# Kernel tuning notes

Hardware: AMD Instinct MI355X
Metric: run time of the kernel (lower is better)

Reference implementation:

```python
import jax, jax.numpy as jnp
import numpy as np

NUM_CLASSES = 19
NUM_PROTO = 10
PROJ_DIM = 720
SK_ITERS = 3
SK_EPS = 0.05
MEAN_GAMMA = 0.999
N = 4 * 128 * 256  # b*h*w = 131072 pixels


def l2n(v, axis=-1):
    return v / jnp.maximum(jnp.linalg.norm(v, axis=axis, keepdims=True), 1e-12)


def layer_norm(v, g, b, eps=1e-5):
    mu = jnp.mean(v, axis=-1, keepdims=True)
    var = jnp.var(v, axis=-1, keepdims=True)
    return (v - mu) / jnp.sqrt(var + eps) * g + b


def _safe_div(a, d):
    return jnp.where(d > 0, a / jnp.where(d > 0, d, 1.0), 0.0)


def setup_inputs() -> dict:
    key = jax.random.key(0)
    k0, k1, k2 = jax.random.split(key, 3)
    x = jax.random.normal(k0, (N, PROJ_DIM), jnp.float32)
    gt_seg = jax.random.randint(k1, (N,), 0, NUM_CLASSES)
    prototypes = 0.02 * jax.random.normal(k2, (NUM_CLASSES, NUM_PROTO, PROJ_DIM), jnp.float32)
    return {
        "x": x,
        "prototypes": prototypes,
        "fn_g": jnp.ones((PROJ_DIM,), jnp.float32),
        "fn_b": jnp.zeros((PROJ_DIM,), jnp.float32),
        "mn_g": jnp.ones((NUM_CLASSES,), jnp.float32),
        "mn_b": jnp.zeros((NUM_CLASSES,), jnp.float32),
        "pn_g": jnp.ones((NUM_CLASSES * NUM_PROTO,), jnp.float32),
        "pn_b": jnp.zeros((NUM_CLASSES * NUM_PROTO,), jnp.float32),
        "gt_seg": gt_seg,
    }


def reference(x, prototypes, fn_g, fn_b, mn_g, mn_b, pn_g, pn_b, gt_seg):
    n = x.shape[0]
    # feat_norm + l2 normalize pixel embeddings; prototypes l2-normalized in-place
    _c = l2n(layer_norm(x, fn_g, fn_b))
    protos = l2n(prototypes)  # [k, m, d]

    # cosine similarity: [n, k, m]
    sim = jnp.einsum("nd,kmd->nkm", _c, protos)
    out_seg = layer_norm(jnp.max(sim, axis=-1), mn_g, mn_b)          # [n, k]
    contrast_logits = layer_norm(sim.reshape(n, -1), pn_g, pn_b)     # [n, k*m]

    # ---- prototype learning (class-masked Sinkhorn, vectorized over classes) ----
    pred = jnp.argmax(out_seg, axis=-1)
    correct = (gt_seg == pred).astype(sim.dtype)                     # [n]
    row_mask = (gt_seg[None, :] == jnp.arange(NUM_CLASSES)[:, None]).astype(sim.dtype)  # [k, n]
    Bk = row_mask.sum(axis=1)                                        # pixels per class

    q0 = jnp.transpose(sim, (1, 0, 2))                               # [k, n, m]
    L = jnp.exp(q0 / SK_EPS) * row_mask[..., None]
    L = _safe_div(L, L.sum(axis=(1, 2), keepdims=True))
    for _ in range(SK_ITERS):
        # normalize over pixels (per prototype), then over prototypes (per pixel)
        L = _safe_div(L, L.sum(axis=1, keepdims=True)) / NUM_PROTO
        L = _safe_div(L, L.sum(axis=2, keepdims=True))
        L = _safe_div(L, Bk[:, None, None])
    L = L * Bk[:, None, None]

    idx = jnp.argmax(L, axis=-1)                                     # [k, n] hard assignment
    onehot = jax.nn.one_hot(idx, NUM_PROTO, dtype=sim.dtype) * row_mask[..., None]
    m_q = onehot * correct[None, :, None]                            # [k, n, m]
    n_km = m_q.sum(axis=1)                                           # [k, m]

    # f = m_q^T @ c_q per class (c_q = _c masked by correct; boolean mask squared == mask)
    f = l2n(jnp.einsum("knm,nd->kmd", m_q, _c))
    valid = (n_km != 0) & (n_km.sum(axis=1, keepdims=True) > 0)      # [k, m]
    updated = MEAN_GAMMA * protos + (1.0 - MEAN_GAMMA) * f
    protos_new = l2n(jnp.where(valid[..., None], updated, protos))

    # proto_target: per-pixel selected prototype offset into the flat codebook
    idx_pix = idx[gt_seg, jnp.arange(n)]
    proto_target = idx_pix.astype(jnp.float32) + NUM_PROTO * gt_seg.astype(jnp.float32)

    return out_seg, contrast_logits, proto_target, protos_new
```

## Files before the change

### kernel.cpp

```cpp
#include <hip/hip_runtime.h>
#include <math.h>

#define NCLS 19
#define NPROTO 10
#define KM 190
#define KMP 192
#define D 720
#define BM 64
#define CHK 16
#define NCHK 45

typedef __bf16 bf16x8 __attribute__((ext_vector_type(8)));
typedef float f32x16 __attribute__((ext_vector_type(16)));

__device__ __forceinline__ float wred_sum(float v) {
#pragma unroll
  for (int o = 32; o > 0; o >>= 1) v += __shfl_xor(v, o, 64);
  return v;
}
__device__ __forceinline__ float wred_max(float v) {
#pragma unroll
  for (int o = 32; o > 0; o >>= 1) v = fmaxf(v, __shfl_xor(v, o, 64));
  return v;
}
__device__ __forceinline__ double wred_sumd(double v) {
#pragma unroll
  for (int o = 32; o > 0; o >>= 1) v += __shfl_xor(v, o, 64);
  return v;
}

__device__ __forceinline__ ushort bf_hi(float v, float& hf) {
  const uint u = __float_as_uint(v);
  const uint r = (u + 0x7FFFu + ((u >> 16) & 1u)) >> 16;
  hf = __uint_as_float(r << 16);
  return (ushort)r;
}

__global__ void prep_gb(const float* __restrict__ fg, const float* __restrict__ fb,
                        float* __restrict__ G2, float* __restrict__ GB,
                        float* __restrict__ C3) {
  const int t = threadIdx.x;
  float cg = 0.f, cgb = 0.f, cb = 0.f;
  for (int d2 = t; d2 < D; d2 += 256) {
    const float g = fg[d2], b = fb[d2];
    G2[d2] = g * g;
    GB[d2] = g * b;
    cg = fmaf(g, g, cg);
    cgb = fmaf(g, b, cgb);
    cb = fmaf(b, b, cb);
  }
  __shared__ float red[3][4];
  cg = wred_sum(cg); cgb = wred_sum(cgb); cb = wred_sum(cb);
  const int w = t >> 6, lane = t & 63;
  if (lane == 0) { red[0][w] = cg; red[1][w] = cgb; red[2][w] = cb; }
  __syncthreads();
  if (t == 0) {
    C3[0] = red[0][0] + red[0][1] + red[0][2] + red[0][3];
    C3[1] = red[1][0] + red[1][1] + red[1][2] + red[1][3];
    C3[2] = red[2][0] + red[2][1] + red[2][2] + red[2][3];
  }
}

__global__ void proto_prep(const float* __restrict__ pr, const float* __restrict__ fg,
                           const float* __restrict__ fb, ushort* __restrict__ pgtb,
                           float* __restrict__ Av, float* __restrict__ Bv) {
  const int j = blockIdx.x, lane = threadIdx.x;
  if (j >= KM) {
#pragma unroll
    for (int jj = 0; jj < 12; ++jj) {
      const int d2 = lane + 64 * jj;
      if (d2 < D) {
        const int c = d2 >> 4, kb = (d2 >> 3) & 1, e = d2 & 7;
        const size_t b0 = (size_t)c * 6144 + (size_t)kb * KMP * 8 + (size_t)j * 8 + e;
        pgtb[b0] = 0;
        pgtb[b0 + 2 * KMP * 8] = 0;
      }
    }
    if (lane == 0) { Av[j] = 0.f; Bv[j] = 0.f; }
    return;
  }
  float pv[12];
  float sp = 0.f;
#pragma unroll
  for (int jj = 0; jj < 12; ++jj) {
    const int d2 = lane + 64 * jj;
    pv[jj] = (d2 < D) ? pr[(size_t)j * D + d2] : 0.f;
    sp = fmaf(pv[jj], pv[jj], sp);
  }
  sp = wred_sum(sp);
  const float ip = 1.f / fmaxf(sqrtf(sp), 1e-12f);
  float sa = 0.f, sb = 0.f;
#pragma unroll
  for (int jj = 0; jj < 12; ++jj) {
    const int d2 = lane + 64 * jj;
    if (d2 < D) {
      const float ph = pv[jj] * ip;
      const float g = fg[d2], b = fb[d2];
      const float val = g * ph;
      float hf, dummy;
      const ushort h = bf_hi(val, hf);
      const ushort l = bf_hi(val - hf, dummy);
      const int c = d2 >> 4, kb = (d2 >> 3) & 1, e = d2 & 7;
      const size_t b0 = (size_t)c * 6144 + (size_t)kb * KMP * 8 + (size_t)j * 8 + e;
      pgtb[b0] = h;
      pgtb[b0 + 2 * KMP * 8] = l;
      sa = fmaf(g, ph, sa);
      sb = fmaf(b, ph, sb);
    }
  }
  sa = wred_sum(sa); sb = wred_sum(sb);
  if (lane == 0) { Av[j] = sa; Bv[j] = sb; }
}

__global__ __launch_bounds__(256, 3) void gemm_main(
    const float* __restrict__ x, const ushort* __restrict__ pgtb,
    const float* __restrict__ Av, const float* __restrict__ Bv,
    const float* __restrict__ G2, const float* __restrict__ GB,
    const float* __restrict__ C3, const int* __restrict__ gt,
    float* __restrict__ out_seg, float* __restrict__ contrast,
    float* __restrict__ se, int* __restrict__ flags,
    const float* __restrict__ mn_g, const float* __restrict__ mn_b,
    const float* __restrict__ pn_g, const float* __restrict__ pn_b, int N) {
  __shared__ __align__(16) union {
    struct {
      ushort X[2][2][2][BM][8];
      ushort P[2][2][2][KMP][8];
    } g;
    float ST[5][4][BM];
    float SIM[BM][KMP];
  } U;
  __shared__ float A_s[KMP], B_s[KMP];
  __shared__ float PGn[KMP], PBn[KMP];
  __shared__ float MGn[32], MBn[32];
  __shared__ float MU[BM], RS[BM], IL[BM];

  const int t = threadIdx.x;
  const int n0 = blockIdx.x * BM;
  const int w = t >> 6, lane = t & 63;
  const int wm = w >> 1, wn = w & 1;
  const int l31 = lane & 31, lhi = lane >> 5;
  const int pix = t & 63, q = t >> 6;

  if (t < KMP) {
    A_s[t] = Av[t]; B_s[t] = Bv[t];
    PGn[t] = (t < KM) ? pn_g[t] : 0.f;
    PBn[t] = (t < KM) ? pn_b[t] : 0.f;
  }
  if (t < NCLS) { MGn[t] = mn_g[t]; MBn[t] = mn_b[t]; }

  f32x16 acc[3];
#pragma unroll
  for (int nt = 0; nt < 3; ++nt)
#pragma unroll
    for (int e = 0; e < 16; ++e) acc[nt][e] = 0.f;

  float s0 = 0.f, qq = 0.f, s1 = 0.f, s2 = 0.f, s3 = 0.f;

  const float* xrow = x + (size_t)(n0 + pix) * D + 4 * q;
  const int kb0 = q >> 1, e0 = (q & 1) * 4;

  auto stageX = [&](int nb, const float4& xv, const float4& g2, const float4& gb) {
    const float vs4[4] = {xv.x, xv.y, xv.z, xv.w};
    const float g2s[4] = {g2.x, g2.y, g2.z, g2.w};
    const float gbs[4] = {gb.x, gb.y, gb.z, gb.w};
    ushort h[4], l[4];
#pragma unroll
    for (int e = 0; e < 4; ++e) {
      const float v = vs4[e];
      float hf, dm;
      h[e] = bf_hi(v, hf);
      l[e] = bf_hi(v - hf, dm);
      s0 += v;
      const float xx = v * v;
      qq += xx;
      s1 = fmaf(v, g2s[e], s1);
      s2 = fmaf(xx, g2s[e], s2);
      s3 = fmaf(v, gbs[e], s3);
    }
    *(ushort4*)&U.g.X[nb][0][kb0][pix][e0] = make_ushort4(h[0], h[1], h[2], h[3]);
    *(ushort4*)&U.g.X[nb][1][kb0][pix][e0] = make_ushort4(l[0], l[1], l[2], l[3]);
  };

  auto mfmaStep = [&](int bf) {
    const int row = 32 * wm + l31;
    const bf16x8 ah = *reinterpret_cast<const bf16x8*>(&U.g.X[bf][0][lhi][row][0]);
    const bf16x8 al = *reinterpret_cast<const bf16x8*>(&U.g.X[bf][1][lhi][row][0]);
    bf16x8 bh[3], bl[3];
#pragma unroll
    for (int nt = 0; nt < 3; ++nt) {
      const int col = 96 * wn + 32 * nt + l31;
      bh[nt] = *reinterpret_cast<const bf16x8*>(&U.g.P[bf][0][lhi][col][0]);
      bl[nt] = *reinterpret_cast<const bf16x8*>(&U.g.P[bf][1][lhi][col][0]);
    }
#pragma unroll
    for (int nt = 0; nt < 3; ++nt)
      acc[nt] = __builtin_amdgcn_mfma_f32_32x32x16_bf16(ah, bh[nt], acc[nt], 0, 0, 0);
#pragma unroll
    for (int nt = 0; nt < 3; ++nt)
      acc[nt] = __builtin_amdgcn_mfma_f32_32x32x16_bf16(ah, bl[nt], acc[nt], 0, 0, 0);
#pragma unroll
    for (int nt = 0; nt < 3; ++nt)
      acc[nt] = __builtin_amdgcn_mfma_f32_32x32x16_bf16(al, bh[nt], acc[nt], 0, 0, 0);
  };

  {
    const uint4* ps = (const uint4*)pgtb;
    const uint4 p0 = ps[t], p1 = ps[t + 256], p2 = ps[t + 512];
    const float4 xv = *(const float4*)xrow;
    const float4 g2 = *(const float4*)&G2[4 * q];
    const float4 gb = *(const float4*)&GB[4 * q];
    uint4* pd = (uint4*)&U.g.P[0][0][0][0][0];
    pd[t] = p0; pd[t + 256] = p1; pd[t + 512] = p2;
    stageX(0, xv, g2, gb);
  }
  __syncthreads();

  for (int c = 0; c < NCHK; ++c) {
    const int buf = c & 1;
    uint4 p0, p1, p2;
    float4 xv, g2, gb;
    const bool pf = (c + 1 < NCHK);
    if (pf) {
      const uint4* ps = (const uint4*)(pgtb + (size_t)(c + 1) * 6144);
      p0 = ps[t]; p1 = ps[t + 256]; p2 = ps[t + 512];
      xv = *(const float4*)(xrow + (c + 1) * CHK);
      const int d0 = (c + 1) * CHK + 4 * q;
      g2 = *(const float4*)&G2[d0];
      gb = *(const float4*)&GB[d0];
    }
    mfmaStep(buf);
    if (pf) {
      uint4* pd = (uint4*)&U.g.P[buf ^ 1][0][0][0][0];
      pd[t] = p0; pd[t + 256] = p1; pd[t + 512] = p2;
      stageX(buf ^ 1, xv, g2, gb);
    }
    __syncthreads();
  }

  U.ST[0][q][pix] = s0;
  U.ST[1][q][pix] = qq;
  U.ST[2][q][pix] = s1;
  U.ST[3][q][pix] = s2;
  U.ST[4][q][pix] = s3;
  __syncthreads();
  if (t < BM) {
    float S0 = 0.f, Q = 0.f, S1 = 0.f, S2 = 0.f, S3 = 0.f;
#pragma unroll
    for (int s = 0; s < 4; ++s) {
      S0 += U.ST[0][s][t];
      Q += U.ST[1][s][t];
      S1 += U.ST[2][s][t];
      S2 += U.ST[3][s][t];
      S3 += U.ST[4][s][t];
    }
    const float Cgg = C3[0], Cgb = C3[1], Cbb = C3[2];
    const float mu = S0 / 720.f;
    const float var = Q / 720.f - mu * mu;
    const float rs = 1.f / sqrtf(var + 1e-5f);
    const float L2v = rs * rs * (S2 - 2.f * mu * S1 + mu * mu * Cgg) +
                      2.f * rs * (S3 - mu * Cgb) + Cbb;
    MU[t] = mu;
    RS[t] = rs;
    IL[t] = 1.f / fmaxf(sqrtf(fmaxf(L2v, 0.f)), 1e-12f);
  }
  __syncthreads();

#pragma unroll
  for (int nt = 0; nt < 3; ++nt) {
    const int col = 96 * wn + 32 * nt + l31;
    const float aC = A_s[col], bC = B_s[col];
#pragma unroll
    for (int rg = 0; rg < 16; ++rg) {
      const int pr = 32 * wm + (rg & 3) + 8 * (rg >> 2) + 4 * lhi;
      U.SIM[pr][col] = (RS[pr] * (acc[nt][rg] - MU[pr] * aC) + bC) * IL[pr];
    }
  }
  __syncthreads();

  const int j0 = lane, j1 = lane + 64, j2 = lane + 128;
  const bool ok2 = (j2 < KM);
  for (int pi = 0; pi < 16; ++pi) {
    const int px = w * 16 + pi;
    const int n = n0 + px;
    const float sv0 = U.SIM[px][j0];
    const float sv1 = U.SIM[px][j1];
    const float sv2 = ok2 ? U.SIM[px][j2] : 0.f;
    float sum = sv0 + sv1 + sv2;
    sum = wred_sum(sum);
    const float mu = sum / 190.f;
    const float d0v = sv0 - mu, d1v = sv1 - mu, d2v = ok2 ? (sv2 - mu) : 0.f;
    float vs = d0v * d0v + d1v * d1v + d2v * d2v;
    vs = wred_sum(vs);
    const float rstd = 1.f / sqrtf(vs / 190.f + 1e-5f);
    contrast[(size_t)n * KM + j0] = d0v * rstd * PGn[j0] + PBn[j0];
    contrast[(size_t)n * KM + j1] = d1v * rstd * PGn[j1] + PBn[j1];
    if (ok2) contrast[(size_t)n * KM + j2] = d2v * rstd * PGn[j2] + PBn[j2];
    const int g0 = gt[n];
    const int b10 = g0 * 10;
    if (j0 >= b10 && j0 < b10 + 10) se[(size_t)n * 10 + (j0 - b10)] = sv0;
    if (j1 >= b10 && j1 < b10 + 10) se[(size_t)n * 10 + (j1 - b10)] = sv1;
    if (ok2 && j2 >= b10 && j2 < b10 + 10) se[(size_t)n * 10 + (j2 - b10)] = sv2;
    float mx = -3.0e38f;
    if (lane < NCLS) {
      const float* row = &U.SIM[px][lane * 10];
#pragma unroll
      for (int m2 = 0; m2 < 10; ++m2) mx = fmaxf(mx, row[m2]);
    }
    float s19 = wred_sum(lane < NCLS ? mx : 0.f);
    const float mu19 = s19 / 19.f;
    const float dv = (lane < NCLS) ? (mx - mu19) : 0.f;
    float v19 = wred_sum(dv * dv);
    const float rs19 = 1.f / sqrtf(v19 / 19.f + 1e-5f);
    float key = -3.0e38f;
    if (lane < NCLS) {
      const float os = dv * rs19 * MGn[lane] + MBn[lane];
      out_seg[(size_t)n * NCLS + lane] = os;
      key = os;
    }
    const float kmax = wred_max(key);
    const unsigned long long bm = __ballot(key == kmax);
    const int pred = __ffsll((unsigned long long)bm) - 1;
    if (lane == 0) flags[n] = (pred == g0) ? 1 : 0;
  }
}

__global__ void sk_colsum(const float* __restrict__ se, const int* __restrict__ gt,
                          const float* __restrict__ u, float* __restrict__ partials,
                          int iter, int nblk, int N) {
  __shared__ float Sl[KMP];
  const int t = threadIdx.x;
  if (t < KMP) Sl[t] = 0.f;
  __syncthreads();
  const int n = blockIdx.x * 256 + t;
  if (n < N) {
    const int b10 = gt[n] * 10;
    float e[10];
#pragma unroll
    for (int m = 0; m < 10; ++m) e[m] = expf(se[(size_t)n * 10 + m] / 0.05f);
    float a = 1.f;
    if (iter > 0) {
      float s = 0.f;
#pragma unroll
      for (int m = 0; m < 10; ++m) s += e[m] * u[b10 + m];
      a = (s > 0.f) ? 1.f / s : 0.f;
    }
#pragma unroll
    for (int m = 0; m < 10; ++m) atomicAdd(&Sl[b10 + m], a * e[m]);
  }
  __syncthreads();
  if (t < KM) partials[(size_t)t * nblk + blockIdx.x] = Sl[t];
}

__global__ void sk_reduce(const float* __restrict__ partials, float* __restrict__ u,
                          int nblk) {
  const int j = blockIdx.x, lane = threadIdx.x;
  double s = 0.0;
  for (int b = lane; b < nblk; b += 64) s += (double)partials[(size_t)j * nblk + b];
  s = wred_sumd(s);
  if (lane == 0) u[j] = (s > 0.0) ? (float)(1.0 / (10.0 * s)) : 0.f;
}

__global__ void sk_final(const float* __restrict__ se, const int* __restrict__ gt,
                         const float* __restrict__ u, const int* __restrict__ flags,
                         float* __restrict__ ptgt, int* __restrict__ list,
                         int* __restrict__ cnt, int* __restrict__ n_km, int N) {
  const int n = blockIdx.x * 256 + threadIdx.x;
  if (n >= N) return;
  const int g0 = gt[n], b10 = g0 * 10;
  float best = -1.f;
  int bi = 0;
#pragma unroll
  for (int m = 0; m < 10; ++m) {
    const float v = expf(se[(size_t)n * 10 + m] / 0.05f) * u[b10 + m];
    if (v > best) { best = v; bi = m; }
  }
  ptgt[n] = (float)(bi + 10 * g0);
  if (flags[n]) {
    atomicAdd(&n_km[b10 + bi], 1);
    const int p = atomicAdd(cnt, 1);
    list[p] = n | (bi << 20) | (g0 << 24);
  }
}

__global__ void f_accum(const float* __restrict__ x, const float* __restrict__ fg,
                        const float* __restrict__ fb, const int* __restrict__ list,
                        const int* __restrict__ cnt, float* __restrict__ f) {
  const int lane = threadIdx.x & 63;
  const int wid = (blockIdx.x * blockDim.x + threadIdx.x) >> 6;
  const int nw = (gridDim.x * blockDim.x) >> 6;
  const int total = *cnt;
  for (int i = wid; i < total; i += nw) {
    const int packed = list[i];
    const int n = packed & 0xFFFFF;
    const int m = (packed >> 20) & 0xF;
    const int k = (packed >> 24) & 0x1F;
    float xv[12];
    float s0 = 0.f, q = 0.f;
#pragma unroll
    for (int jj = 0; jj < 12; ++jj) {
      const int d2 = lane + 64 * jj;
      xv[jj] = (d2 < D) ? x[(size_t)n * D + d2] : 0.f;
      s0 += xv[jj];
      q = fmaf(xv[jj], xv[jj], q);
    }
    s0 = wred_sum(s0);
    q = wred_sum(q);
    const float mu = s0 / 720.f;
    const float var = q / 720.f - mu * mu;
    const float rs = 1.f / sqrtf(var + 1e-5f);
    float cv[12];
    float l2 = 0.f;
#pragma unroll
    for (int jj = 0; jj < 12; ++jj) {
      const int d2 = lane + 64 * jj;
      if (d2 < D) {
        cv[jj] = (xv[jj] - mu) * rs * fg[d2] + fb[d2];
        l2 = fmaf(cv[jj], cv[jj], l2);
      } else {
        cv[jj] = 0.f;
      }
    }
    l2 = wred_sum(l2);
    const float il = 1.f / fmaxf(sqrtf(l2), 1e-12f);
    float* frow = &f[(size_t)(k * 10 + m) * D];
#pragma unroll
    for (int jj = 0; jj < 12; ++jj) {
      const int d2 = lane + 64 * jj;
      if (d2 < D) atomicAdd(&frow[d2], cv[jj] * il);
    }
  }
}

__global__ void protos_out(const float* __restrict__ pr, const float* __restrict__ f,
                           const int* __restrict__ n_km, float* __restrict__ out) {
  const int j = blockIdx.x, lane = threadIdx.x;
  float pv[12], fv[12];
  float sp = 0.f, sf = 0.f;
#pragma unroll
  for (int jj = 0; jj < 12; ++jj) {
    const int d2 = lane + 64 * jj;
    pv[jj] = (d2 < D) ? pr[(size_t)j * D + d2] : 0.f;
    fv[jj] = (d2 < D) ? f[(size_t)j * D + d2] : 0.f;
    sp = fmaf(pv[jj], pv[jj], sp);
    sf = fmaf(fv[jj], fv[jj], sf);
  }
  sp = wred_sum(sp);
  sf = wred_sum(sf);
  const float ip = 1.f / fmaxf(sqrtf(sp), 1e-12f);
  const float iff = 1.f / fmaxf(sqrtf(sf), 1e-12f);
  const bool valid = n_km[j] > 0;
  float vv[12];
  float sv = 0.f;
#pragma unroll
  for (int jj = 0; jj < 12; ++jj) {
    const float ph = pv[jj] * ip;
    vv[jj] = valid ? (0.999f * ph + 0.001f * (fv[jj] * iff)) : ph;
    sv = fmaf(vv[jj], vv[jj], sv);
  }
  sv = wred_sum(sv);
  const float ivv = 1.f / fmaxf(sqrtf(sv), 1e-12f);
#pragma unroll
  for (int jj = 0; jj < 12; ++jj) {
    const int d2 = lane + 64 * jj;
    if (d2 < D) out[(size_t)j * D + d2] = vv[jj] * ivv;
  }
}

extern "C" void kernel_launch(void* const* d_in, const int* in_sizes, int n_in,
                              void* d_out, int out_size, void* d_ws, size_t ws_size,
                              hipStream_t stream) {
  const float* x = (const float*)d_in[0];
  const float* protos = (const float*)d_in[1];
  const float* fn_g = (const float*)d_in[2];
  const float* fn_b = (const float*)d_in[3];
  const float* mn_g = (const float*)d_in[4];
  const float* mn_b = (const float*)d_in[5];
  const float* pn_g = (const float*)d_in[6];
  const float* pn_b = (const float*)d_in[7];
  const int* gt = (const int*)d_in[8];
  const int N = in_sizes[0] / D;

  float* out_seg = (float*)d_out;
  float* contrast = out_seg + (size_t)N * NCLS;
  float* ptgt = contrast + (size_t)N * KM;
  float* pnew = ptgt + (size_t)N;

  char* ws = (char*)d_ws;
  size_t off = 0;
  auto alloc = [&](size_t bytes) {
    char* p = ws + off;
    off = (off + bytes + 255) & ~(size_t)255;
    return p;
  };
  const int nblk = (N + 255) / 256;
  ushort* pgtb = (ushort*)alloc((size_t)NCHK * 6144 * 2);
  float* Av = (float*)alloc(KMP * 4);
  float* Bv = (float*)alloc(KMP * 4);
  float* G2 = (float*)alloc(D * 4);
  float* GB = (float*)alloc(D * 4);
  float* C3 = (float*)alloc(4 * 4);
  float* se = (float*)alloc((size_t)N * 10 * 4);
  float* partials = (float*)alloc((size_t)KM * nblk * 4);
  float* u = (float*)alloc(KMP * 4);
  float* f = (float*)alloc((size_t)KM * D * 4);
  int* n_km = (int*)alloc(KMP * 4);
  int* flags = (int*)alloc((size_t)N * 4);
  int* list = (int*)alloc((size_t)N * 4);
  int* cnt = (int*)alloc(256);

  hipMemsetAsync(f, 0, (size_t)KM * D * 4, stream);
  hipMemsetAsync(n_km, 0, KMP * 4, stream);
  hipMemsetAsync(cnt, 0, 4, stream);

  prep_gb<<<1, 256, 0, stream>>>(fn_g, fn_b, G2, GB, C3);
  proto_prep<<<KMP, 64, 0, stream>>>(protos, fn_g, fn_b, pgtb, Av, Bv);
  gemm_main<<<N / BM, 256, 0, stream>>>(x, pgtb, Av, Bv, G2, GB, C3, gt, out_seg,
                                        contrast, se, flags, mn_g, mn_b, pn_g,
                                        pn_b, N);
  for (int it = 0; it < 3; ++it) {
    sk_colsum<<<nblk, 256, 0, stream>>>(se, gt, u, partials, it, nblk, N);
    sk_reduce<<<KM, 64, 0, stream>>>(partials, u, nblk);
  }
  sk_final<<<nblk, 256, 0, stream>>>(se, gt, u, flags, ptgt, list, cnt, n_km, N);
  f_accum<<<256, 256, 0, stream>>>(x, fn_g, fn_b, list, cnt, f);
  protos_out<<<KM, 64, 0, stream>>>(protos, f, n_km, pnew);
}
```

Baseline: 861.5 us.

## Restructure pipeline: larger GEMM tile, split epilogue, fused Sinkhorn and prototype update

The GEMM tile grows to 128 rows per block with two accumulator row groups per warp, and the similarity matrix is written straight to global memory instead of being staged in shared memory. The layer-norm epilogue moves into a separate kernel that reads those rows back. The Sinkhorn colsum/reduce/final launches are merged into one per-class kernel with 1024 threads, and f_accum plus protos_out become a single per-prototype gather kernel that reuses stored per-pixel mu/rstd/inverse-norm values. This cuts launch count, atomics and the recomputation of x statistics, but adds an extra global round trip of the 190-wide similarity rows. It also leaves only 19 blocks for the Sinkhorn passes, each scanning all of gt.

```diff
diff --git a/kernel.cpp b/kernel.cpp
--- a/kernel.cpp
+++ b/kernel.cpp
@@ -6,7 +6,7 @@
 #define KM 190
 #define KMP 192
 #define D 720
-#define BM 64
+#define BM 128
 #define CHK 16
 #define NCHK 45
 
@@ -36,35 +36,30 @@
   return (ushort)r;
 }
 
-__global__ void prep_gb(const float* __restrict__ fg, const float* __restrict__ fb,
-                        float* __restrict__ G2, float* __restrict__ GB,
-                        float* __restrict__ C3) {
-  const int t = threadIdx.x;
-  float cg = 0.f, cgb = 0.f, cb = 0.f;
-  for (int d2 = t; d2 < D; d2 += 256) {
-    const float g = fg[d2], b = fb[d2];
-    G2[d2] = g * g;
-    GB[d2] = g * b;
-    cg = fmaf(g, g, cg);
-    cgb = fmaf(g, b, cgb);
-    cb = fmaf(b, b, cb);
-  }
-  __shared__ float red[3][4];
-  cg = wred_sum(cg); cgb = wred_sum(cgb); cb = wred_sum(cb);
-  const int w = t >> 6, lane = t & 63;
-  if (lane == 0) { red[0][w] = cg; red[1][w] = cgb; red[2][w] = cb; }
-  __syncthreads();
-  if (t == 0) {
-    C3[0] = red[0][0] + red[0][1] + red[0][2] + red[0][3];
-    C3[1] = red[1][0] + red[1][1] + red[1][2] + red[1][3];
-    C3[2] = red[2][0] + red[2][1] + red[2][2] + red[2][3];
-  }
-}
-
-__global__ void proto_prep(const float* __restrict__ pr, const float* __restrict__ fg,
-                           const float* __restrict__ fb, ushort* __restrict__ pgtb,
-                           float* __restrict__ Av, float* __restrict__ Bv) {
+__global__ void prep_all(const float* __restrict__ pr, const float* __restrict__ fg,
+                         const float* __restrict__ fb, ushort* __restrict__ pgtb,
+                         float* __restrict__ Av, float* __restrict__ Bv,
+                         float* __restrict__ G2, float* __restrict__ GB,
+                         float* __restrict__ C3) {
   const int j = blockIdx.x, lane = threadIdx.x;
+  if (j == KMP) {
+    float cg = 0.f, cgb = 0.f, cb = 0.f;
+#pragma unroll
+    for (int jj = 0; jj < 12; ++jj) {
+      const int d2 = lane + 64 * jj;
+      if (d2 < D) {
+        const float g = fg[d2], b = fb[d2];
+        G2[d2] = g * g;
+        GB[d2] = g * b;
+        cg = fmaf(g, g, cg);
+        cgb = fmaf(g, b, cgb);
+        cb = fmaf(b, b, cb);
+      }
+    }
+    cg = wred_sum(cg); cgb = wred_sum(cgb); cb = wred_sum(cb);
+    if (lane == 0) { C3[0] = cg; C3[1] = cgb; C3[2] = cb; }
+    return;
+  }
   if (j >= KM) {
 #pragma unroll
     for (int jj = 0; jj < 12; ++jj) {
@@ -116,22 +111,17 @@
     const float* __restrict__ x, const ushort* __restrict__ pgtb,
     const float* __restrict__ Av, const float* __restrict__ Bv,
     const float* __restrict__ G2, const float* __restrict__ GB,
-    const float* __restrict__ C3, const int* __restrict__ gt,
-    float* __restrict__ out_seg, float* __restrict__ contrast,
-    float* __restrict__ se, int* __restrict__ flags,
-    const float* __restrict__ mn_g, const float* __restrict__ mn_b,
-    const float* __restrict__ pn_g, const float* __restrict__ pn_b, int N) {
+    const float* __restrict__ C3, float* __restrict__ simC,
+    float* __restrict__ MUg, float* __restrict__ RSg, float* __restrict__ ILg,
+    int N) {
   __shared__ __align__(16) union {
     struct {
       ushort X[2][2][2][BM][8];
       ushort P[2][2][2][KMP][8];
     } g;
-    float ST[5][4][BM];
-    float SIM[BM][KMP];
+    float ST[5][2][BM];
   } U;
   __shared__ float A_s[KMP], B_s[KMP];
-  __shared__ float PGn[KMP], PBn[KMP];
-  __shared__ float MGn[32], MBn[32];
   __shared__ float MU[BM], RS[BM], IL[BM];
 
   const int t = threadIdx.x;
@@ -139,170 +129,189 @@
   const int w = t >> 6, lane = t & 63;
   const int wm = w >> 1, wn = w & 1;
   const int l31 = lane & 31, lhi = lane >> 5;
-  const int pix = t & 63, q = t >> 6;
-
-  if (t < KMP) {
-    A_s[t] = Av[t]; B_s[t] = Bv[t];
-    PGn[t] = (t < KM) ? pn_g[t] : 0.f;
-    PBn[t] = (t < KM) ? pn_b[t] : 0.f;
-  }
-  if (t < NCLS) { MGn[t] = mn_g[t]; MBn[t] = mn_b[t]; }
-
-  f32x16 acc[3];
-#pragma unroll
-  for (int nt = 0; nt < 3; ++nt)
-#pragma unroll
-    for (int e = 0; e < 16; ++e) acc[nt][e] = 0.f;
+  const int p = t & 127, h = t >> 7;
+
+  if (t < KMP) { A_s[t] = Av[t]; B_s[t] = Bv[t]; }
+
+  f32x16 acc[2][3];
+#pragma unroll
+  for (int mr = 0; mr < 2; ++mr)
+#pragma unroll
+    for (int nt = 0; nt < 3; ++nt)
+#pragma unroll
+      for (int e = 0; e < 16; ++e) acc[mr][nt][e] = 0.f;
 
   float s0 = 0.f, qq = 0.f, s1 = 0.f, s2 = 0.f, s3 = 0.f;
 
-  const float* xrow = x + (size_t)(n0 + pix) * D + 4 * q;
-  const int kb0 = q >> 1, e0 = (q & 1) * 4;
-
-  auto stageX = [&](int nb, const float4& xv, const float4& g2, const float4& gb) {
-    const float vs4[4] = {xv.x, xv.y, xv.z, xv.w};
-    const float g2s[4] = {g2.x, g2.y, g2.z, g2.w};
-    const float gbs[4] = {gb.x, gb.y, gb.z, gb.w};
-    ushort h[4], l[4];
-#pragma unroll
-    for (int e = 0; e < 4; ++e) {
-      const float v = vs4[e];
+  const float* xrow = x + (size_t)(n0 + p) * D + 8 * h;
+
+  auto stageX = [&](int nb, int c, const float4& xa, const float4& xb) {
+    const int d0 = c * CHK + 8 * h;
+    const float4 g2a = *(const float4*)&G2[d0];
+    const float4 g2b = *(const float4*)&G2[d0 + 4];
+    const float4 gba = *(const float4*)&GB[d0];
+    const float4 gbb = *(const float4*)&GB[d0 + 4];
+    const float v[8] = {xa.x, xa.y, xa.z, xa.w, xb.x, xb.y, xb.z, xb.w};
+    const float gg[8] = {g2a.x, g2a.y, g2a.z, g2a.w, g2b.x, g2b.y, g2b.z, g2b.w};
+    const float gv[8] = {gba.x, gba.y, gba.z, gba.w, gbb.x, gbb.y, gbb.z, gbb.w};
+    ushort hh[8], ll[8];
+#pragma unroll
+    for (int e = 0; e < 8; ++e) {
+      const float xv = v[e];
       float hf, dm;
-      h[e] = bf_hi(v, hf);
-      l[e] = bf_hi(v - hf, dm);
-      s0 += v;
-      const float xx = v * v;
+      hh[e] = bf_hi(xv, hf);
+      ll[e] = bf_hi(xv - hf, dm);
+      s0 += xv;
+      const float xx = xv * xv;
       qq += xx;
-      s1 = fmaf(v, g2s[e], s1);
-      s2 = fmaf(xx, g2s[e], s2);
-      s3 = fmaf(v, gbs[e], s3);
-    }
-    *(ushort4*)&U.g.X[nb][0][kb0][pix][e0] = make_ushort4(h[0], h[1], h[2], h[3]);
-    *(ushort4*)&U.g.X[nb][1][kb0][pix][e0] = make_ushort4(l[0], l[1], l[2], l[3]);
+      s1 = fmaf(xv, gg[e], s1);
+      s2 = fmaf(xx, gg[e], s2);
+      s3 = fmaf(xv, gv[e], s3);
+    }
+    *(uint4*)&U.g.X[nb][0][h][p][0] =
+        make_uint4((uint)hh[0] | ((uint)hh[1] << 16), (uint)hh[2] | ((uint)hh[3] << 16),
+                   (uint)hh[4] | ((uint)hh[5] << 16), (uint)hh[6] | ((uint)hh[7] << 16));
+    *(uint4*)&U.g.X[nb][1][h][p][0] =
+        make_uint4((uint)ll[0] | ((uint)ll[1] << 16), (uint)ll[2] | ((uint)ll[3] << 16),
+                   (uint)ll[4] | ((uint)ll[5] << 16), (uint)ll[6] | ((uint)ll[7] << 16));
   };
 
   auto mfmaStep = [&](int bf) {
-    const int row = 32 * wm + l31;
-    const bf16x8 ah = *reinterpret_cast<const bf16x8*>(&U.g.X[bf][0][lhi][row][0]);
-    const bf16x8 al = *reinterpret_cast<const bf16x8*>(&U.g.X[bf][1][lhi][row][0]);
-    bf16x8 bh[3], bl[3];
+    const int row0 = 64 * wm + l31;
+    const bf16x8 ah0 = *reinterpret_cast<const bf16x8*>(&U.g.X[bf][0][lhi][row0][0]);
+    const bf16x8 ah1 = *reinterpret_cast<const bf16x8*>(&U.g.X[bf][0][lhi][row0 + 32][0]);
+    const bf16x8 al0 = *reinterpret_cast<const bf16x8*>(&U.g.X[bf][1][lhi][row0][0]);
+    const bf16x8 al1 = *reinterpret_cast<const bf16x8*>(&U.g.X[bf][1][lhi][row0 + 32][0]);
 #pragma unroll
     for (int nt = 0; nt < 3; ++nt) {
       const int col = 96 * wn + 32 * nt + l31;
-      bh[nt] = *reinterpret_cast<const bf16x8*>(&U.g.P[bf][0][lhi][col][0]);
-      bl[nt] = *reinterpret_cast<const bf16x8*>(&U.g.P[bf][1][lhi][col][0]);
-    }
-#pragma unroll
-    for (int nt = 0; nt < 3; ++nt)
-      acc[nt] = __builtin_amdgcn_mfma_f32_32x32x16_bf16(ah, bh[nt], acc[nt], 0, 0, 0);
-#pragma unroll
-    for (int nt = 0; nt < 3; ++nt)
-      acc[nt] = __builtin_amdgcn_mfma_f32_32x32x16_bf16(ah, bl[nt], acc[nt], 0, 0, 0);
-#pragma unroll
-    for (int nt = 0; nt < 3; ++nt)
-      acc[nt] = __builtin_amdgcn_mfma_f32_32x32x16_bf16(al, bh[nt], acc[nt], 0, 0, 0);
+      const bf16x8 bh = *reinterpret_cast<const bf16x8*>(&U.g.P[bf][0][lhi][col][0]);
+      const bf16x8 bl = *reinterpret_cast<const bf16x8*>(&U.g.P[bf][1][lhi][col][0]);
+      acc[0][nt] = __builtin_amdgcn_mfma_f32_32x32x16_bf16(ah0, bh, acc[0][nt], 0, 0, 0);
+      acc[1][nt] = __builtin_amdgcn_mfma_f32_32x32x16_bf16(ah1, bh, acc[1][nt], 0, 0, 0);
+      acc[0][nt] = __builtin_amdgcn_mfma_f32_32x32x16_bf16(ah0, bl, acc[0][nt], 0, 0, 0);
+      acc[1][nt] = __builtin_amdgcn_mfma_f32_32x32x16_bf16(ah1, bl, acc[1][nt], 0, 0, 0);
+      acc[0][nt] = __builtin_amdgcn_mfma_f32_32x32x16_bf16(al0, bh, acc[0][nt], 0, 0, 0);
+      acc[1][nt] = __builtin_amdgcn_mfma_f32_32x32x16_bf16(al1, bh, acc[1][nt], 0, 0, 0);
+    }
   };
 
   {
     const uint4* ps = (const uint4*)pgtb;
     const uint4 p0 = ps[t], p1 = ps[t + 256], p2 = ps[t + 512];
-    const float4 xv = *(const float4*)xrow;
-    const float4 g2 = *(const float4*)&G2[4 * q];
-    const float4 gb = *(const float4*)&GB[4 * q];
+    const float4 xa = *(const float4*)xrow;
+    const float4 xb = *(const float4*)(xrow + 4);
     uint4* pd = (uint4*)&U.g.P[0][0][0][0][0];
     pd[t] = p0; pd[t + 256] = p1; pd[t + 512] = p2;
-    stageX(0, xv, g2, gb);
+    stageX(0, 0, xa, xb);
   }
   __syncthreads();
 
   for (int c = 0; c < NCHK; ++c) {
     const int buf = c & 1;
+    const bool pf = (c + 1 < NCHK);
     uint4 p0, p1, p2;
-    float4 xv, g2, gb;
-    const bool pf = (c + 1 < NCHK);
+    float4 xa, xb;
     if (pf) {
       const uint4* ps = (const uint4*)(pgtb + (size_t)(c + 1) * 6144);
       p0 = ps[t]; p1 = ps[t + 256]; p2 = ps[t + 512];
-      xv = *(const float4*)(xrow + (c + 1) * CHK);
-      const int d0 = (c + 1) * CHK + 4 * q;
-      g2 = *(const float4*)&G2[d0];
-      gb = *(const float4*)&GB[d0];
+      xa = *(const float4*)(xrow + (c + 1) * CHK);
+      xb = *(const float4*)(xrow + (c + 1) * CHK + 4);
     }
     mfmaStep(buf);
     if (pf) {
       uint4* pd = (uint4*)&U.g.P[buf ^ 1][0][0][0][0];
       pd[t] = p0; pd[t + 256] = p1; pd[t + 512] = p2;
-      stageX(buf ^ 1, xv, g2, gb);
+      stageX(buf ^ 1, c + 1, xa, xb);
     }
     __syncthreads();
   }
 
-  U.ST[0][q][pix] = s0;
-  U.ST[1][q][pix] = qq;
-  U.ST[2][q][pix] = s1;
-  U.ST[3][q][pix] = s2;
-  U.ST[4][q][pix] = s3;
+  U.ST[0][h][p] = s0;
+  U.ST[1][h][p] = qq;
+  U.ST[2][h][p] = s1;
+  U.ST[3][h][p] = s2;
+  U.ST[4][h][p] = s3;
   __syncthreads();
   if (t < BM) {
-    float S0 = 0.f, Q = 0.f, S1 = 0.f, S2 = 0.f, S3 = 0.f;
-#pragma unroll
-    for (int s = 0; s < 4; ++s) {
-      S0 += U.ST[0][s][t];
-      Q += U.ST[1][s][t];
-      S1 += U.ST[2][s][t];
-      S2 += U.ST[3][s][t];
-      S3 += U.ST[4][s][t];
-    }
+    const float S0 = U.ST[0][0][t] + U.ST[0][1][t];
+    const float Q = U.ST[1][0][t] + U.ST[1][1][t];
+    const float S1 = U.ST[2][0][t] + U.ST[2][1][t];
+    const float S2 = U.ST[3][0][t] + U.ST[3][1][t];
+    const float S3 = U.ST[4][0][t] + U.ST[4][1][t];
     const float Cgg = C3[0], Cgb = C3[1], Cbb = C3[2];
     const float mu = S0 / 720.f;
     const float var = Q / 720.f - mu * mu;
     const float rs = 1.f / sqrtf(var + 1e-5f);
     const float L2v = rs * rs * (S2 - 2.f * mu * S1 + mu * mu * Cgg) +
                       2.f * rs * (S3 - mu * Cgb) + Cbb;
-    MU[t] = mu;
-    RS[t] = rs;
-    IL[t] = 1.f / fmaxf(sqrtf(fmaxf(L2v, 0.f)), 1e-12f);
+    const float il = 1.f / fmaxf(sqrtf(fmaxf(L2v, 0.f)), 1e-12f);
+    MU[t] = mu; RS[t] = rs; IL[t] = il;
+    MUg[n0 + t] = mu; RSg[n0 + t] = rs; ILg[n0 + t] = il;
   }
   __syncthreads();
 
+  float aC[3], bC[3];
 #pragma unroll
   for (int nt = 0; nt < 3; ++nt) {
     const int col = 96 * wn + 32 * nt + l31;
-    const float aC = A_s[col], bC = B_s[col];
+    aC[nt] = A_s[col];
+    bC[nt] = B_s[col];
+  }
+#pragma unroll
+  for (int mr = 0; mr < 2; ++mr)
 #pragma unroll
     for (int rg = 0; rg < 16; ++rg) {
-      const int pr = 32 * wm + (rg & 3) + 8 * (rg >> 2) + 4 * lhi;
-      U.SIM[pr][col] = (RS[pr] * (acc[nt][rg] - MU[pr] * aC) + bC) * IL[pr];
-    }
-  }
+      const int r = 64 * wm + 32 * mr + (rg & 3) + 8 * (rg >> 2) + 4 * lhi;
+      const float mu = MU[r], rs = RS[r], il = IL[r];
+#pragma unroll
+      for (int nt = 0; nt < 3; ++nt) {
+        const int col = 96 * wn + 32 * nt + l31;
+        if (col < KM)
+          simC[(size_t)(n0 + r) * KM + col] =
+              (rs * (acc[mr][nt][rg] - mu * aC[nt]) + bC[nt]) * il;
+      }
+    }
+}
+
+__global__ __launch_bounds__(256) void epilogue(
+    float* __restrict__ co, const int* __restrict__ gt,
+    float* __restrict__ out_seg, float* __restrict__ se, int* __restrict__ flags,
+    const float* __restrict__ mn_g, const float* __restrict__ mn_b,
+    const float* __restrict__ pn_g, const float* __restrict__ pn_b, int N) {
+  __shared__ float PGn[KMP], PBn[KMP], MGn[32], MBn[32];
+  __shared__ float rowbuf[4][KMP];
+  const int t = threadIdx.x, w = t >> 6, lane = t & 63;
+  if (t < KM) { PGn[t] = pn_g[t]; PBn[t] = pn_b[t]; }
+  if (t < NCLS) { MGn[t] = mn_g[t]; MBn[t] = mn_b[t]; }
   __syncthreads();
-
+  const int n0 = blockIdx.x * 64;
   const int j0 = lane, j1 = lane + 64, j2 = lane + 128;
   const bool ok2 = (j2 < KM);
   for (int pi = 0; pi < 16; ++pi) {
-    const int px = w * 16 + pi;
-    const int n = n0 + px;
-    const float sv0 = U.SIM[px][j0];
-    const float sv1 = U.SIM[px][j1];
-    const float sv2 = ok2 ? U.SIM[px][j2] : 0.f;
-    float sum = sv0 + sv1 + sv2;
-    sum = wred_sum(sum);
+    const int n = n0 + w * 16 + pi;
+    float* crow = &co[(size_t)n * KM];
+    const float sv0 = crow[j0];
+    const float sv1 = crow[j1];
+    const float sv2 = ok2 ? crow[j2] : 0.f;
+    float sum = wred_sum(sv0 + sv1 + sv2);
     const float mu = sum / 190.f;
     const float d0v = sv0 - mu, d1v = sv1 - mu, d2v = ok2 ? (sv2 - mu) : 0.f;
-    float vs = d0v * d0v + d1v * d1v + d2v * d2v;
-    vs = wred_sum(vs);
+    float vs = wred_sum(d0v * d0v + d1v * d1v + d2v * d2v);
     const float rstd = 1.f / sqrtf(vs / 190.f + 1e-5f);
-    contrast[(size_t)n * KM + j0] = d0v * rstd * PGn[j0] + PBn[j0];
-    contrast[(size_t)n * KM + j1] = d1v * rstd * PGn[j1] + PBn[j1];
-    if (ok2) contrast[(size_t)n * KM + j2] = d2v * rstd * PGn[j2] + PBn[j2];
-    const int g0 = gt[n];
-    const int b10 = g0 * 10;
+    rowbuf[w][j0] = sv0;
+    rowbuf[w][j1] = sv1;
+    if (ok2) rowbuf[w][j2] = sv2;
+    const int g0 = gt[n], b10 = g0 * 10;
     if (j0 >= b10 && j0 < b10 + 10) se[(size_t)n * 10 + (j0 - b10)] = sv0;
     if (j1 >= b10 && j1 < b10 + 10) se[(size_t)n * 10 + (j1 - b10)] = sv1;
     if (ok2 && j2 >= b10 && j2 < b10 + 10) se[(size_t)n * 10 + (j2 - b10)] = sv2;
+    crow[j0] = d0v * rstd * PGn[j0] + PBn[j0];
+    crow[j1] = d1v * rstd * PGn[j1] + PBn[j1];
+    if (ok2) crow[j2] = d2v * rstd * PGn[j2] + PBn[j2];
     float mx = -3.0e38f;
     if (lane < NCLS) {
-      const float* row = &U.SIM[px][lane * 10];
+      const float* row = &rowbuf[w][lane * 10];
 #pragma unroll
       for (int m2 = 0; m2 < 10; ++m2) mx = fmaxf(mx, row[m2]);
     }
@@ -324,146 +333,139 @@
   }
 }
 
-__global__ void sk_colsum(const float* __restrict__ se, const int* __restrict__ gt,
-                          const float* __restrict__ u, float* __restrict__ partials,
-                          int iter, int nblk, int N) {
-  __shared__ float Sl[KMP];
-  const int t = threadIdx.x;
-  if (t < KMP) Sl[t] = 0.f;
+__global__ __launch_bounds__(1024) void sk_all(
+    const float* __restrict__ se, const int* __restrict__ gt,
+    const int* __restrict__ flags, float* __restrict__ ptgt,
+    int* __restrict__ list, int* __restrict__ cnt, int N) {
+  const int k = blockIdx.x;
+  const int t = threadIdx.x, w = t >> 6, lane = t & 63;
+  __shared__ double CS[16][10];
+  __shared__ float u_s[10];
+  for (int pass = 0; pass < 3; ++pass) {
+    double cs[10];
+#pragma unroll
+    for (int m = 0; m < 10; ++m) cs[m] = 0.0;
+    for (int n = t; n < N; n += 1024) {
+      if (gt[n] != k) continue;
+      float e[10];
+      const float2* sp2 = (const float2*)&se[(size_t)n * 10];
+#pragma unroll
+      for (int m2 = 0; m2 < 5; ++m2) {
+        const float2 v = sp2[m2];
+        e[2 * m2] = expf(v.x / 0.05f);
+        e[2 * m2 + 1] = expf(v.y / 0.05f);
+      }
+      float a = 1.f;
+      if (pass > 0) {
+        float s = 0.f;
+#pragma unroll
+        for (int m = 0; m < 10; ++m) s += e[m] * u_s[m];
+        a = (s > 0.f) ? 1.f / s : 0.f;
+      }
+#pragma unroll
+      for (int m = 0; m < 10; ++m) cs[m] += (double)(a * e[m]);
+    }
+#pragma unroll
+    for (int m = 0; m < 10; ++m) cs[m] = wred_sumd(cs[m]);
+    if (lane == 0)
+#pragma unroll
+      for (int m = 0; m < 10; ++m) CS[w][m] = cs[m];
+    __syncthreads();
+    if (t < 10) {
+      double s = 0.0;
+#pragma unroll
+      for (int ww = 0; ww < 16; ++ww) s += CS[ww][t];
+      u_s[t] = (s > 0.0) ? (float)(1.0 / (10.0 * s)) : 0.f;
+    }
+    __syncthreads();
+  }
+  for (int n = t; n < N; n += 1024) {
+    if (gt[n] != k) continue;
+    float best = -1.f;
+    int bi = 0;
+#pragma unroll
+    for (int m = 0; m < 10; ++m) {
+      const float v = expf(se[(size_t)n * 10 + m] / 0.05f) * u_s[m];
+      if (v > best) { best = v; bi = m; }
+    }
+    ptgt[n] = (float)(bi + 10 * k);
+    if (flags[n]) {
+      const int pos = atomicAdd(cnt, 1);
+      list[pos] = n | (bi << 20) | (k << 24);
+    }
+  }
+}
+
+__global__ __launch_bounds__(256) void proto_update(
+    const float* __restrict__ pr, const float* __restrict__ x,
+    const float* __restrict__ fg, const float* __restrict__ fb,
+    const float* __restrict__ MUg, const float* __restrict__ RSg,
+    const float* __restrict__ ILg, const int* __restrict__ list,
+    const int* __restrict__ cnt, float* __restrict__ out) {
+  const int j = blockIdx.x;
+  const int t = threadIdx.x, w = t >> 6, lane = t & 63;
+  const int tag = ((j / 10) << 4) | (j % 10);
+  const int d0 = t, d1 = t + 256, d2 = t + 512;
+  const bool has2 = (d2 < D);
+  const float fg0 = fg[d0], fb0 = fb[d0];
+  const float fg1 = fg[d1], fb1 = fb[d1];
+  const float fg2 = has2 ? fg[d2] : 0.f, fb2 = has2 ? fb[d2] : 0.f;
+  float fa0 = 0.f, fa1 = 0.f, fa2 = 0.f;
+  __shared__ int nlist[4096];
+  __shared__ int nmatch;
+  __shared__ float RP[4], RF[4], RV[4];
+  const int total = *cnt;
+  int hits = 0;
+  for (int base = 0; base < total; base += 4096) {
+    const int hi = min(base + 4096, total);
+    if (t == 0) nmatch = 0;
+    __syncthreads();
+    for (int i = base + t; i < hi; i += 256) {
+      const int pk = list[i];
+      if ((pk >> 20) == tag) {
+        const int pos = atomicAdd(&nmatch, 1);
+        nlist[pos] = pk & 0xFFFFF;
+      }
+    }
+    __syncthreads();
+    const int nm = nmatch;
+    hits += nm;
+    for (int ii = 0; ii < nm; ++ii) {
+      const int n = nlist[ii];
+      const float mu = MUg[n], rs = RSg[n], il = ILg[n];
+      const float* xr = &x[(size_t)n * D];
+      fa0 += ((xr[d0] - mu) * rs * fg0 + fb0) * il;
+      fa1 += ((xr[d1] - mu) * rs * fg1 + fb1) * il;
+      if (has2) fa2 += ((xr[d2] - mu) * rs * fg2 + fb2) * il;
+    }
+    __syncthreads();
+  }
+  const float pv0 = pr[(size_t)j * D + d0];
+  const float pv1 = pr[(size_t)j * D + d1];
+  const float pv2 = has2 ? pr[(size_t)j * D + d2] : 0.f;
+  float sp = pv0 * pv0 + pv1 * pv1 + pv2 * pv2;
+  float sf = fa0 * fa0 + fa1 * fa1 + fa2 * fa2;
+  sp = wred_sum(sp); sf = wred_sum(sf);
+  if (lane == 0) { RP[w] = sp; RF[w] = sf; }
   __syncthreads();
-  const int n = blockIdx.x * 256 + t;
-  if (n < N) {
-    const int b10 = gt[n] * 10;
-    float e[10];
-#pragma unroll
-    for (int m = 0; m < 10; ++m) e[m] = expf(se[(size_t)n * 10 + m] / 0.05f);
-    float a = 1.f;
-    if (iter > 0) {
-      float s = 0.f;
-#pragma unroll
-      for (int m = 0; m < 10; ++m) s += e[m] * u[b10 + m];
-      a = (s > 0.f) ? 1.f / s : 0.f;
-    }
-#pragma unroll
-    for (int m = 0; m < 10; ++m) atomicAdd(&Sl[b10 + m], a * e[m]);
-  }
-  __syncthreads();
-  if (t < KM) partials[(size_t)t * nblk + blockIdx.x] = Sl[t];
-}
-
-__global__ void sk_reduce(const float* __restrict__ partials, float* __restrict__ u,
-                          int nblk) {
-  const int j = blockIdx.x, lane = threadIdx.x;
-  double s = 0.0;
-  for (int b = lane; b < nblk; b += 64) s += (double)partials[(size_t)j * nblk + b];
-  s = wred_sumd(s);
-  if (lane == 0) u[j] = (s > 0.0) ? (float)(1.0 / (10.0 * s)) : 0.f;
-}
-
-__global__ void sk_final(const float* __restrict__ se, const int* __restrict__ gt,
-                         const float* __restrict__ u, const int* __restrict__ flags,
-                         float* __restrict__ ptgt, int* __restrict__ list,
-                         int* __restrict__ cnt, int* __restrict__ n_km, int N) {
-  const int n = blockIdx.x * 256 + threadIdx.x;
-  if (n >= N) return;
-  const int g0 = gt[n], b10 = g0 * 10;
-  float best = -1.f;
-  int bi = 0;
-#pragma unroll
-  for (int m = 0; m < 10; ++m) {
-    const float v = expf(se[(size_t)n * 10 + m] / 0.05f) * u[b10 + m];
-    if (v > best) { best = v; bi = m; }
-  }
-  ptgt[n] = (float)(bi + 10 * g0);
-  if (flags[n]) {
-    atomicAdd(&n_km[b10 + bi], 1);
-    const int p = atomicAdd(cnt, 1);
-    list[p] = n | (bi << 20) | (g0 << 24);
-  }
-}
-
-__global__ void f_accum(const float* __restrict__ x, const float* __restrict__ fg,
-                        const float* __restrict__ fb, const int* __restrict__ list,
-                        const int* __restrict__ cnt, float* __restrict__ f) {
-  const int lane = threadIdx.x & 63;
-  const int wid = (blockIdx.x * blockDim.x + threadIdx.x) >> 6;
-  const int nw = (gridDim.x * blockDim.x) >> 6;
-  const int total = *cnt;
-  for (int i = wid; i < total; i += nw) {
-    const int packed = list[i];
-    const int n = packed & 0xFFFFF;
-    const int m = (packed >> 20) & 0xF;
-    const int k = (packed >> 24) & 0x1F;
-    float xv[12];
-    float s0 = 0.f, q = 0.f;
-#pragma unroll
-    for (int jj = 0; jj < 12; ++jj) {
-      const int d2 = lane + 64 * jj;
-      xv[jj] = (d2 < D) ? x[(size_t)n * D + d2] : 0.f;
-      s0 += xv[jj];
-      q = fmaf(xv[jj], xv[jj], q);
-    }
-    s0 = wred_sum(s0);
-    q = wred_sum(q);
-    const float mu = s0 / 720.f;
-    const float var = q / 720.f - mu * mu;
-    const float rs = 1.f / sqrtf(var + 1e-5f);
-    float cv[12];
-    float l2 = 0.f;
-#pragma unroll
-    for (int jj = 0; jj < 12; ++jj) {
-      const int d2 = lane + 64 * jj;
-      if (d2 < D) {
-        cv[jj] = (xv[jj] - mu) * rs * fg[d2] + fb[d2];
-        l2 = fmaf(cv[jj], cv[jj], l2);
-      } else {
-        cv[jj] = 0.f;
-      }
-    }
-    l2 = wred_sum(l2);
-    const float il = 1.f / fmaxf(sqrtf(l2), 1e-12f);
-    float* frow = &f[(size_t)(k * 10 + m) * D];
-#pragma unroll
-    for (int jj = 0; jj < 12; ++jj) {
-      const int d2 = lane + 64 * jj;
-      if (d2 < D) atomicAdd(&frow[d2], cv[jj] * il);
-    }
-  }
-}
-
-__global__ void protos_out(const float* __restrict__ pr, const float* __restrict__ f,
-                           const int* __restrict__ n_km, float* __restrict__ out) {
-  const int j = blockIdx.x, lane = threadIdx.x;
-  float pv[12], fv[12];
-  float sp = 0.f, sf = 0.f;
-#pragma unroll
-  for (int jj = 0; jj < 12; ++jj) {
-    const int d2 = lane + 64 * jj;
-    pv[jj] = (d2 < D) ? pr[(size_t)j * D + d2] : 0.f;
-    fv[jj] = (d2 < D) ? f[(size_t)j * D + d2] : 0.f;
-    sp = fmaf(pv[jj], pv[jj], sp);
-    sf = fmaf(fv[jj], fv[jj], sf);
-  }
-  sp = wred_sum(sp);
-  sf = wred_sum(sf);
+  sp = RP[0] + RP[1] + RP[2] + RP[3];
+  sf = RF[0] + RF[1] + RF[2] + RF[3];
   const float ip = 1.f / fmaxf(sqrtf(sp), 1e-12f);
   const float iff = 1.f / fmaxf(sqrtf(sf), 1e-12f);
-  const bool valid = n_km[j] > 0;
-  float vv[12];
-  float sv = 0.f;
-#pragma unroll
-  for (int jj = 0; jj < 12; ++jj) {
-    const float ph = pv[jj] * ip;
-    vv[jj] = valid ? (0.999f * ph + 0.001f * (fv[jj] * iff)) : ph;
-    sv = fmaf(vv[jj], vv[jj], sv);
-  }
+  const bool valid = hits > 0;
+  const float ph0 = pv0 * ip, ph1 = pv1 * ip, ph2 = pv2 * ip;
+  const float vv0 = valid ? 0.999f * ph0 + 0.001f * (fa0 * iff) : ph0;
+  const float vv1 = valid ? 0.999f * ph1 + 0.001f * (fa1 * iff) : ph1;
+  const float vv2 = valid ? 0.999f * ph2 + 0.001f * (fa2 * iff) : ph2;
+  float sv = vv0 * vv0 + vv1 * vv1 + vv2 * vv2;
   sv = wred_sum(sv);
+  if (lane == 0) RV[w] = sv;
+  __syncthreads();
+  sv = RV[0] + RV[1] + RV[2] + RV[3];
   const float ivv = 1.f / fmaxf(sqrtf(sv), 1e-12f);
-#pragma unroll
-  for (int jj = 0; jj < 12; ++jj) {
-    const int d2 = lane + 64 * jj;
-    if (d2 < D) out[(size_t)j * D + d2] = vv[jj] * ivv;
-  }
+  out[(size_t)j * D + d0] = vv0 * ivv;
+  out[(size_t)j * D + d1] = vv1 * ivv;
+  if (has2) out[(size_t)j * D + d2] = vv2 * ivv;
 }
 
 extern "C" void kernel_launch(void* const* d_in, const int* in_sizes, int n_in,
@@ -492,7 +494,6 @@
     off = (off + bytes + 255) & ~(size_t)255;
     return p;
   };
-  const int nblk = (N + 255) / 256;
   ushort* pgtb = (ushort*)alloc((size_t)NCHK * 6144 * 2);
   float* Av = (float*)alloc(KMP * 4);
   float* Bv = (float*)alloc(KMP * 4);
@@ -500,28 +501,21 @@
   float* GB = (float*)alloc(D * 4);
   float* C3 = (float*)alloc(4 * 4);
   float* se = (float*)alloc((size_t)N * 10 * 4);
-  float* partials = (float*)alloc((size_t)KM * nblk * 4);
-  float* u = (float*)alloc(KMP * 4);
-  float* f = (float*)alloc((size_t)KM * D * 4);
-  int* n_km = (int*)alloc(KMP * 4);
+  float* MUg = (float*)alloc((size_t)N * 4);
+  float* RSg = (float*)alloc((size_t)N * 4);
+  float* ILg = (float*)alloc((size_t)N * 4);
   int* flags = (int*)alloc((size_t)N * 4);
   int* list = (int*)alloc((size_t)N * 4);
   int* cnt = (int*)alloc(256);
 
-  hipMemsetAsync(f, 0, (size_t)KM * D * 4, stream);
-  hipMemsetAsync(n_km, 0, KMP * 4, stream);
   hipMemsetAsync(cnt, 0, 4, stream);
 
-  prep_gb<<<1, 256, 0, stream>>>(fn_g, fn_b, G2, GB, C3);
-  proto_prep<<<KMP, 64, 0, stream>>>(protos, fn_g, fn_b, pgtb, Av, Bv);
-  gemm_main<<<N / BM, 256, 0, stream>>>(x, pgtb, Av, Bv, G2, GB, C3, gt, out_seg,
-                                        contrast, se, flags, mn_g, mn_b, pn_g,
-                                        pn_b, N);
-  for (int it = 0; it < 3; ++it) {
-    sk_colsum<<<nblk, 256, 0, stream>>>(se, gt, u, partials, it, nblk, N);
-    sk_reduce<<<KM, 64, 0, stream>>>(partials, u, nblk);
-  }
-  sk_final<<<nblk, 256, 0, stream>>>(se, gt, u, flags, ptgt, list, cnt, n_km, N);
-  f_accum<<<256, 256, 0, stream>>>(x, fn_g, fn_b, list, cnt, f);
-  protos_out<<<KM, 64, 0, stream>>>(protos, f, n_km, pnew);
-}
+  prep_all<<<KMP + 1, 64, 0, stream>>>(protos, fn_g, fn_b, pgtb, Av, Bv, G2, GB, C3);
+  gemm_main<<<N / BM, 256, 0, stream>>>(x, pgtb, Av, Bv, G2, GB, C3, contrast,
+                                        MUg, RSg, ILg, N);
+  epilogue<<<N / 64, 256, 0, stream>>>(contrast, gt, out_seg, se, flags, mn_g,
+                                       mn_b, pn_g, pn_b, N);
+  sk_all<<<NCLS, 1024, 0, stream>>>(se, gt, flags, ptgt, list, cnt, N);
+  proto_update<<<KM, 256, 0, stream>>>(protos, x, fn_g, fn_b, MUg, RSg, ILg,
+                                       list, cnt, pnew);
+}
```

Result: slower. 2.097 ms (+143.5%).
